# Performance work log

Measured on AMD Instinct MI355X. Metric: run time of the kernel, lower is better.

Reference implementation:

```python
import jax, jax.numpy as jnp
import numpy as np

OUT_DIM = 130

def _gru_cell(x, h, wih, whh, bih, bhh):
    # torch.nn.GRUCell math
    gi = x @ wih.T + bih            # [N, 3H]
    gh = h @ whh.T + bhh            # [N, 3H]
    ir, iz, inn = jnp.split(gi, 3, axis=-1)
    hr, hz, hn = jnp.split(gh, 3, axis=-1)
    r = jax.nn.sigmoid(ir + hr)
    z = jax.nn.sigmoid(iz + hz)
    n = jnp.tanh(inn + r * hn)
    return (1.0 - z) * n + z * h


def setup_inputs() -> dict:
    key = jax.random.key(0)
    ks = jax.random.split(key, 16)
    E, B, C, H, D = 16, 128, 512, 1024, OUT_DIM
    S = 16  # length // 2
    T = E * S
    s = 0.02
    inp = {
        "c": jax.random.normal(ks[0], (E, B, C), jnp.float32),
        "target": jax.random.normal(ks[1], (B, T, D), jnp.float32),
        "length": 32,
        "batch_size": B,
        "fc_init_w": s * jax.random.normal(ks[2], (2 * H, C), jnp.float32),
        "fc_init_b": s * jax.random.normal(ks[3], (2 * H,), jnp.float32),
        "g1_wih": s * jax.random.normal(ks[4], (3 * H, C + D), jnp.float32),
        "g1_whh": s * jax.random.normal(ks[5], (3 * H, H), jnp.float32),
        "g1_bih": s * jax.random.normal(ks[6], (3 * H,), jnp.float32),
        "g1_bhh": s * jax.random.normal(ks[7], (3 * H,), jnp.float32),
        "g2_wih": s * jax.random.normal(ks[8], (3 * H, H), jnp.float32),
        "g2_whh": s * jax.random.normal(ks[9], (3 * H, H), jnp.float32),
        "g2_bih": s * jax.random.normal(ks[10], (3 * H,), jnp.float32),
        "g2_bhh": s * jax.random.normal(ks[11], (3 * H,), jnp.float32),
        "fco_w": s * jax.random.normal(ks[12], (D, H), jnp.float32),
        "fco_b": s * jax.random.normal(ks[13], (D,), jnp.float32),
    }
    return inp


def reference(c, target, length, batch_size, fc_init_w, fc_init_b,
              g1_wih, g1_whh, g1_bih, g1_bhh,
              g2_wih, g2_whh, g2_bih, g2_bhh, fco_w, fco_b):
    E, B, C = c.shape
    H = fc_init_w.shape[0] // 2
    D = fco_w.shape[0]
    S = length // 2
    T = E * S
    # h1/h2 init per conductor embed: tanh(fc_init(embed))
    t0 = jnp.tanh(c @ fc_init_w.T + fc_init_b)           # [E,B,2H]
    h1 = t0[..., :H].reshape(E * B, H)
    h2 = t0[..., H:].reshape(E * B, H)
    # teacher-forced previous: prev[t]=0 at t=0 else target[:,t-1]
    prev = jnp.concatenate([jnp.zeros((B, 1, D), target.dtype), target[:, :T - 1]], axis=1)  # [B,T,D]
    # global step t = e*S + s -> [S, E*B, D]
    prev = prev.transpose(1, 0, 2).reshape(E, S, B, D).transpose(1, 0, 2, 3).reshape(S, E * B, D)
    cflat = c.reshape(E * B, C)

    def step(carry, prev_t):
        h1, h2 = carry
        x = jnp.concatenate([cflat, prev_t], axis=-1)    # [E*B, C+D]
        h1 = _gru_cell(x, h1, g1_wih, g1_whh, g1_bih, g1_bhh)
        h2 = _gru_cell(h1, h2, g2_wih, g2_whh, g2_bih, g2_bhh)
        y = h2 @ fco_w.T + fco_b                         # [E*B, D]
        return (h1, h2), y

    _, ys = jax.lax.scan(step, (h1, h2), prev)           # [S, E*B, D]
    ys = ys.reshape(S, E, B, D).transpose(2, 1, 0, 3).reshape(B, T, D)
    return ys
```

## Files before the change

kernel.cpp:

```cpp
#include <hip/hip_runtime.h>

typedef unsigned short u16;
typedef __attribute__((ext_vector_type(8))) short frag8;
typedef __attribute__((ext_vector_type(4))) float f32x4;
typedef __attribute__((ext_vector_type(8))) unsigned short u16x8;

typedef __attribute__((address_space(1))) const void GV;
typedef __attribute__((address_space(3))) void LV;

__device__ __forceinline__ void gl16(const u16* g, u16* l) {
  __builtin_amdgcn_global_load_lds((GV*)g, (LV*)l, 16, 0, 0);
}

__device__ __forceinline__ float b2f(u16 u) {
  union { unsigned int i; float f; } v; v.i = ((unsigned int)u) << 16; return v.f;
}
__device__ __forceinline__ u16 f2b(float f) {
  union { float f; unsigned int i; } v; v.f = f;
  unsigned int x = v.i;
  x += 0x7fffu + ((x >> 16) & 1u);
  return (u16)(x >> 16);
}
__device__ __forceinline__ float ftanh(float x) {
  float e = __expf(2.f * x);
  return 1.f - 2.f / (e + 1.f);
}

__device__ __forceinline__ void xcd_remap(int axis, int& bx, int& by) {
  const int nx = gridDim.x, ny = gridDim.y;
  const int nwg = nx * ny;
  const int bid = blockIdx.x + nx * blockIdx.y;
  const int q = nwg >> 3, r = nwg & 7;
  const int xcd = bid & 7, i = bid >> 3;
  const int rem = (xcd < r ? xcd * (q + 1) : r * (q + 1) + (xcd - r) * q) + i;
  if (axis == 0) { bx = rem / ny; by = rem - bx * ny; }
  else           { by = rem / nx; bx = rem - by * nx; }
}

__global__ void mega_prep(const float* __restrict__ c, const float* __restrict__ fiw,
                          const float* __restrict__ g1whh, const float* __restrict__ g2wih,
                          const float* __restrict__ g2whh, const float* __restrict__ g1wih,
                          const float* __restrict__ fcow, const float* __restrict__ target,
                          u16* __restrict__ cbf, u16* __restrict__ Wfi, u16* __restrict__ W1h,
                          u16* __restrict__ W2i, u16* __restrict__ W2h, u16* __restrict__ Wc,
                          u16* __restrict__ Wd, u16* __restrict__ WBy, u16* __restrict__ P)
{
  int i = blockIdx.x * 256 + threadIdx.x;
  if (i < 1048576) { cbf[i] = f2b(c[i]); return; }
  i -= 1048576;
  if (i < 1048576) { Wfi[i] = f2b(fiw[i]); return; }
  i -= 1048576;
  if (i < 3145728) { W1h[i] = f2b(g1whh[i]); return; }
  i -= 3145728;
  if (i < 3145728) { W2i[i] = f2b(g2wih[i]); return; }
  i -= 3145728;
  if (i < 3145728) { W2h[i] = f2b(g2whh[i]); return; }
  i -= 3145728;
  if (i < 1572864) { int n = i >> 9, k = i & 511; Wc[i] = f2b(g1wih[n * 642 + k]); return; }
  i -= 1572864;
  if (i < 589824) {
    int n = i / 192, k = i - n * 192;
    Wd[i] = (k < 130) ? f2b(g1wih[n * 642 + 512 + k]) : (u16)0;
    return;
  }
  i -= 589824;
  if (i < 262144) { int n = i >> 10; WBy[i] = (n < 130) ? f2b(fcow[i]) : (u16)0; return; }
  i -= 262144;
  {
    int row = i / 24;
    int k0 = (i - row * 24) * 8;
    int t = row >> 11, m2 = row & 2047;
    int e = m2 >> 7, b = m2 & 127;
    int tt = e * 16 + t;
    u16x8 r;
    if (tt > 0 && k0 + 8 <= 130) {
      const float* trow = target + (size_t)(b * 256 + tt - 1) * 130 + k0;
#pragma unroll
      for (int q = 0; q < 8; ++q) r[q] = f2b(trow[q]);
    } else if (tt > 0 && k0 < 130) {
      const float* trow = target + (size_t)(b * 256 + tt - 1) * 130;
#pragma unroll
      for (int q = 0; q < 8; ++q) { int k = k0 + q; r[q] = (k < 130) ? f2b(trow[k]) : (u16)0; }
    } else {
#pragma unroll
      for (int q = 0; q < 8; ++q) r[q] = (u16)0;
    }
    *(u16x8*)&P[(size_t)row * 192 + k0] = r;
  }
}

__device__ __forceinline__ void kloop3(
    const u16* gA, const u16* gB, int nk,
    u16* AsBase, u16* BsBase, int wave,
    int rdA, int rdB, f32x4 (&acc)[2][4])
{
  u16* Adst = AsBase + wave * 512;
  u16* Bdst = BsBase + wave * 512;
  gl16(gA,      Adst);        gl16(gB,      Bdst);
  gl16(gA + 32, Adst + 4096); gl16(gB + 32, Bdst + 4096);
  const u16* pA = gA + 64;
  const u16* pB = gB + 64;
  int cbuf = 0, nbuf = 2;
  for (int ks = 0; ks < nk; ++ks) {
    if (ks < nk - 1) asm volatile("s_waitcnt vmcnt(2)" : : : "memory");
    else             asm volatile("s_waitcnt vmcnt(0)" : : : "memory");
    __builtin_amdgcn_s_barrier();
    __builtin_amdgcn_sched_barrier(0);
    if (ks + 2 < nk) {
      gl16(pA, Adst + nbuf * 4096);
      gl16(pB, Bdst + nbuf * 4096);
      pA += 32; pB += 32;
    }
    const u16* Ab = AsBase + cbuf * 4096;
    const u16* Bb = BsBase + cbuf * 4096;
    frag8 af[2], bfr[4];
#pragma unroll
    for (int i = 0; i < 2; ++i)
      af[i] = *(const frag8*)&Ab[rdA + i * 512];
#pragma unroll
    for (int j = 0; j < 4; ++j)
      bfr[j] = *(const frag8*)&Bb[rdB + j * 512];
#pragma unroll
    for (int i = 0; i < 2; ++i)
#pragma unroll
      for (int j = 0; j < 4; ++j)
        acc[i][j] = __builtin_amdgcn_mfma_f32_16x16x32_bf16(af[i], bfr[j], acc[i][j], 0, 0, 0);
    cbuf = (cbuf == 2) ? 0 : cbuf + 1;
    nbuf = (nbuf == 2) ? 0 : nbuf + 1;
  }
}

struct GeomT { int wave, lane, wm, wn, lr, lq, rdA, rdB, srow, scol; };
__device__ __forceinline__ GeomT geom(int tid) {
  GeomT g;
  g.wave = tid >> 6; g.lane = tid & 63;
  g.wm = (g.wave & 3) * 32; g.wn = (g.wave >> 2) * 64;
  g.lr = g.lane & 15; g.lq = g.lane >> 4;
  int sw = (g.lr >> 1) & 3;
  g.rdA = (g.wm + g.lr) * 32 + ((g.lq ^ sw) << 3);
  g.rdB = (g.wn + g.lr) * 32 + ((g.lq ^ sw) << 3);
  g.srow = g.wave * 16 + (g.lane >> 2);
  g.scol = (((g.lane & 3) ^ ((g.lane >> 3) & 3)) << 3);
  return g;
}

__global__ __launch_bounds__(512, 6) void gemm_bt(
    const u16* __restrict__ A, int lda,
    const u16* __restrict__ B0, const u16* __restrict__ B1, int ldb, int n_split,
    int N, int K, int mode, int tstep, int axis,
    const float* __restrict__ bias0, const float* __restrict__ bias1,
    u16* __restrict__ out0, u16* __restrict__ out1,
    const u16* __restrict__ addmat,
    float* __restrict__ fout0, float* __restrict__ fout1)
{
  __shared__ u16 As[3 * 4096];
  __shared__ u16 Bs[3 * 4096];
  int bx, by; xcd_remap(axis, bx, by);
  GeomT g = geom(threadIdx.x);
  const int m0 = by * 128, n0 = bx * 128;

  const u16* Bsel; int nb0;
  if (n0 < n_split) { Bsel = B0; nb0 = n0; }
  else              { Bsel = B1; nb0 = n0 - n_split; }

  f32x4 acc[2][4] = {};
  const u16* gA = &A[(size_t)(m0 + g.srow) * lda + g.scol];
  const u16* gB = &Bsel[(size_t)(nb0 + g.srow) * ldb + g.scol];
  kloop3(gA, gB, K >> 5, As, Bs, g.wave, g.rdA, g.rdB, acc);

#pragma unroll
  for (int i = 0; i < 2; ++i) {
#pragma unroll
    for (int r = 0; r < 4; ++r) {
      int m = m0 + g.wm + i * 16 + g.lq * 4 + r;
#pragma unroll
      for (int j = 0; j < 4; ++j) {
        int n = n0 + g.wn + j * 16 + g.lr;
        float v = acc[i][j][r];
        if (mode == 2) {
          out0[(size_t)m * 3072 + n] = f2b(v + b2f(addmat[(size_t)(m & 2047) * 3072 + n]));
        } else if (mode == 3) {
          if (n < 3072) out0[(size_t)m * 3072 + n] = f2b(v + bias0[n]);
          else          out1[(size_t)m * 3072 + (n - 3072)] = f2b(v + bias1[n - 3072]);
        } else {
          if (n < 3072) {
            out0[(size_t)m * 3072 + n] = f2b(v + bias0[n]);
          } else if (n < 3202) {
            int d = n - 3072;
            int b = m & 127, e = m >> 7;
            fout0[(size_t)((b << 8) + (e << 4) + tstep) * 130 + d] = v + bias1[d];
          }
        }
      }
    }
  }
}

__global__ __launch_bounds__(512, 6) void gemm_A(
    const u16* __restrict__ cbf, const u16* __restrict__ Wfi, const u16* __restrict__ Wc,
    const float* __restrict__ fib, const float* __restrict__ g1bih,
    float* __restrict__ h1f, float* __restrict__ h2f,
    u16* __restrict__ h1b, u16* __restrict__ h2b, u16* __restrict__ gic)
{
  __shared__ u16 As[3 * 4096];
  __shared__ u16 Bs[3 * 4096];
  int bx, by; xcd_remap(0, bx, by);
  GeomT g = geom(threadIdx.x);
  const int m0 = by * 128;
  const int isInit = (bx < 16);
  const int nb0 = isInit ? bx * 128 : (bx - 16) * 128;
  const u16* Bw = isInit ? Wfi : Wc;

  f32x4 acc[2][4] = {};
  const u16* gA = &cbf[(size_t)(m0 + g.srow) * 512 + g.scol];
  const u16* gB = &Bw[(size_t)(nb0 + g.srow) * 512 + g.scol];
  kloop3(gA, gB, 16, As, Bs, g.wave, g.rdA, g.rdB, acc);

#pragma unroll
  for (int i = 0; i < 2; ++i) {
#pragma unroll
    for (int r = 0; r < 4; ++r) {
      int m = m0 + g.wm + i * 16 + g.lq * 4 + r;
#pragma unroll
      for (int j = 0; j < 4; ++j) {
        int n = nb0 + g.wn + j * 16 + g.lr;
        float v = acc[i][j][r];
        if (isInit) {
          float t = ftanh(v + fib[n]);
          if (n < 1024) { h1f[(size_t)m * 1024 + n] = t;          h1b[(size_t)m * 1024 + n] = f2b(t); }
          else          { h2f[(size_t)m * 1024 + (n - 1024)] = t; h2b[(size_t)m * 1024 + (n - 1024)] = f2b(t); }
        } else {
          gic[(size_t)m * 3072 + n] = f2b(v + g1bih[n]);
        }
      }
    }
  }
}

__global__ __launch_bounds__(512, 6) void gemm_B(
    const u16* __restrict__ h1b, const u16* __restrict__ h2b, const u16* __restrict__ P,
    const u16* __restrict__ W1h, const u16* __restrict__ W2h, const u16* __restrict__ Wd,
    const float* __restrict__ b1hh, const float* __restrict__ b2hh,
    const u16* __restrict__ gic,
    u16* __restrict__ gh1, u16* __restrict__ gh2, u16* __restrict__ gi1w)
{
  __shared__ u16 As[3 * 4096];
  __shared__ u16 Bs[3 * 4096];
  int bx, by; xcd_remap(0, bx, by);
  GeomT g = geom(threadIdx.x);
  const int m0 = by * 128;
  int reg, nb0;
  const u16 *A, *Bw; int ld, K;
  if (bx < 24)      { reg = 0; nb0 = bx * 128;        A = h1b; Bw = W1h; ld = 1024; K = 1024; }
  else if (bx < 48) { reg = 1; nb0 = (bx - 24) * 128; A = h2b; Bw = W2h; ld = 1024; K = 1024; }
  else              { reg = 2; nb0 = (bx - 48) * 128; A = P;   Bw = Wd;  ld = 192;  K = 192;  }

  f32x4 acc[2][4] = {};
  const u16* gA = &A[(size_t)(m0 + g.srow) * ld + g.scol];
  const u16* gB = &Bw[(size_t)(nb0 + g.srow) * ld + g.scol];
  kloop3(gA, gB, K >> 5, As, Bs, g.wave, g.rdA, g.rdB, acc);

#pragma unroll
  for (int i = 0; i < 2; ++i) {
#pragma unroll
    for (int r = 0; r < 4; ++r) {
      int m = m0 + g.wm + i * 16 + g.lq * 4 + r;
#pragma unroll
      for (int j = 0; j < 4; ++j) {
        int n = nb0 + g.wn + j * 16 + g.lr;
        float v = acc[i][j][r];
        if (reg == 0)      gh1[(size_t)m * 3072 + n] = f2b(v + b1hh[n]);
        else if (reg == 1) gh2[(size_t)m * 3072 + n] = f2b(v + b2hh[n]);
        else               gi1w[(size_t)m * 3072 + n] = f2b(v + b2f(gic[(size_t)m * 3072 + n]));
      }
    }
  }
}

__global__ __launch_bounds__(512, 6) void gemm_fused(
    const u16* __restrict__ h1b, const u16* __restrict__ h2b, const u16* __restrict__ Pt,
    const u16* __restrict__ W2i, const u16* __restrict__ W1h, const u16* __restrict__ W2h,
    const u16* __restrict__ WBy, const u16* __restrict__ Wd,
    const float* __restrict__ b_gi2, const float* __restrict__ b_gh1,
    const float* __restrict__ b_gh2, const float* __restrict__ b_y,
    const u16* __restrict__ gic,
    u16* __restrict__ gi2, u16* __restrict__ gh1, u16* __restrict__ gh2,
    float* __restrict__ y, u16* __restrict__ gi1w,
    int c0, int c1, int c2, int c3, int tstep)
{
  __shared__ u16 As[3 * 4096];
  __shared__ u16 Bs[3 * 4096];
  int bx, by; xcd_remap(0, bx, by);
  GeomT g = geom(threadIdx.x);
  const int m0 = by * 128;
  int reg, nb0;
  const u16 *A, *Bw; int ld, K;
  if (bx < c0)      { reg = 0; nb0 = bx * 128;        A = h1b; Bw = W2i; ld = 1024; K = 1024; }
  else if (bx < c1) { reg = 1; nb0 = (bx - c0) * 128; A = h1b; Bw = W1h; ld = 1024; K = 1024; }
  else if (bx < c2) { reg = 2; nb0 = (bx - c1) * 128; A = h2b; Bw = W2h; ld = 1024; K = 1024; }
  else if (bx < c3) { reg = 3; nb0 = (bx - c2) * 128; A = h2b; Bw = WBy; ld = 1024; K = 1024; }
  else              { reg = 4; nb0 = (bx - c3) * 128; A = Pt;  Bw = Wd;  ld = 192;  K = 192;  }

  f32x4 acc[2][4] = {};
  const u16* gA = &A[(size_t)(m0 + g.srow) * ld + g.scol];
  const u16* gB = &Bw[(size_t)(nb0 + g.srow) * ld + g.scol];
  kloop3(gA, gB, K >> 5, As, Bs, g.wave, g.rdA, g.rdB, acc);

#pragma unroll
  for (int i = 0; i < 2; ++i) {
#pragma unroll
    for (int r = 0; r < 4; ++r) {
      int m = m0 + g.wm + i * 16 + g.lq * 4 + r;
#pragma unroll
      for (int j = 0; j < 4; ++j) {
        int nl = nb0 + g.wn + j * 16 + g.lr;
        float v = acc[i][j][r];
        if (reg == 0)      gi2[(size_t)m * 3072 + nl] = f2b(v + b_gi2[nl]);
        else if (reg == 1) gh1[(size_t)m * 3072 + nl] = f2b(v + b_gh1[nl]);
        else if (reg == 2) gh2[(size_t)m * 3072 + nl] = f2b(v + b_gh2[nl]);
        else if (reg == 3) {
          if (nl < 130) {
            int b = m & 127, e = m >> 7;
            y[(size_t)((b << 8) + (e << 4) + tstep) * 130 + nl] = v + b_y[nl];
          }
        } else {
          gi1w[(size_t)m * 3072 + nl] = f2b(v + b2f(gic[(size_t)m * 3072 + nl]));
        }
      }
    }
  }
}

__global__ __launch_bounds__(256) void gru2(
    const u16* __restrict__ giA, const u16* __restrict__ ghA,
    float* __restrict__ hA, u16* __restrict__ hbA,
    const u16* __restrict__ giB, const u16* __restrict__ ghB,
    float* __restrict__ hB, u16* __restrict__ hbB,
    int doA, int doB)
{
  int blk = blockIdx.x;
  const u16 *gi, *gh; float* h32; u16* hb16;
  if (blk < 1024) { if (!doA) return; gi = giA; gh = ghA; h32 = hA; hb16 = hbA; }
  else { if (!doB) return; gi = giB; gh = ghB; h32 = hB; hb16 = hbB; blk -= 1024; }
  int idx = blk * 256 + threadIdx.x;
  int m = idx >> 7;
  int j0 = (idx & 127) << 3;
  const size_t gb = (size_t)m * 3072 + j0;
  const size_t hb = (size_t)m * 1024 + j0;
  u16x8 ir = *(const u16x8*)&gi[gb];
  u16x8 iz = *(const u16x8*)&gi[gb + 1024];
  u16x8 in_ = *(const u16x8*)&gi[gb + 2048];
  u16x8 hr = *(const u16x8*)&gh[gb];
  u16x8 hz = *(const u16x8*)&gh[gb + 1024];
  u16x8 hn = *(const u16x8*)&gh[gb + 2048];
  f32x4 h0 = *(const f32x4*)&h32[hb];
  f32x4 h1v = *(const f32x4*)&h32[hb + 4];
  f32x4 o0, o1;
  u16x8 ob;
#pragma unroll
  for (int q = 0; q < 8; ++q) {
    float r = 1.f / (1.f + __expf(-(b2f(ir[q]) + b2f(hr[q]))));
    float z = 1.f / (1.f + __expf(-(b2f(iz[q]) + b2f(hz[q]))));
    float nn = ftanh(b2f(in_[q]) + r * b2f(hn[q]));
    float hh = (q < 4) ? h0[q & 3] : h1v[q & 3];
    float res = (1.f - z) * nn + z * hh;
    if (q < 4) o0[q & 3] = res; else o1[q & 3] = res;
    ob[q] = f2b(res);
  }
  *(f32x4*)&h32[hb] = o0;
  *(f32x4*)&h32[hb + 4] = o1;
  *(u16x8*)&hb16[hb] = ob;
}

extern "C" void kernel_launch(void* const* d_in, const int* in_sizes, int n_in,
                              void* d_out, int out_size, void* d_ws, size_t ws_size,
                              hipStream_t stream)
{
  const float* c      = (const float*)d_in[0];
  const float* target = (const float*)d_in[1];
  const float* fiw    = (const float*)d_in[4];
  const float* fib    = (const float*)d_in[5];
  const float* g1wih  = (const float*)d_in[6];
  const float* g1whh  = (const float*)d_in[7];
  const float* g1bih  = (const float*)d_in[8];
  const float* g1bhh  = (const float*)d_in[9];
  const float* g2wih  = (const float*)d_in[10];
  const float* g2whh  = (const float*)d_in[11];
  const float* g2bih  = (const float*)d_in[12];
  const float* g2bhh  = (const float*)d_in[13];
  const float* fcow   = (const float*)d_in[14];
  const float* fcob   = (const float*)d_in[15];
  float* out = (float*)d_out;

  char* wsp = (char*)d_ws;
  size_t off = 0;
  auto takeb = [&](size_t bytes) {
    void* p = (void*)(wsp + off);
    off += bytes;
    off = (off + 255) & ~(size_t)255;
    return p;
  };
  float* h1f = (float*)takeb((size_t)2048 * 1024 * 4);
  float* h2f = (float*)takeb((size_t)2048 * 1024 * 4);
  u16* h1b   = (u16*)takeb((size_t)2048 * 1024 * 2);
  u16* h2b   = (u16*)takeb((size_t)2048 * 1024 * 2);
  u16* gic   = (u16*)takeb((size_t)2048 * 3072 * 2);
  u16* gib   = (u16*)takeb((size_t)2048 * 3072 * 2);
  u16* gh1   = (u16*)takeb((size_t)2048 * 3072 * 2);
  u16* gh2   = (u16*)takeb((size_t)2048 * 3072 * 2);
  u16* cbf   = (u16*)takeb((size_t)2048 * 512 * 2);
  u16* Wfi   = (u16*)takeb((size_t)2048 * 512 * 2);
  u16* Wc    = (u16*)takeb((size_t)3072 * 512 * 2);
  u16* Wd    = (u16*)takeb((size_t)3072 * 192 * 2);
  u16* W1h   = (u16*)takeb((size_t)3072 * 1024 * 2);
  u16* W2i   = (u16*)takeb((size_t)3072 * 1024 * 2);
  u16* W2h   = (u16*)takeb((size_t)3072 * 1024 * 2);
  u16* WBy   = (u16*)takeb((size_t)256 * 1024 * 2);
  u16* P     = (u16*)takeb((size_t)32768 * 192 * 2);
  u16* g1A = nullptr;
  if (ws_size >= off + (size_t)2048 * 3072 * 2 + 256) g1A = (u16*)takeb((size_t)2048 * 3072 * 2);
  (void)in_sizes; (void)n_in; (void)out_size;

  const int BIG = 1 << 30;

  mega_prep<<<57600, 256, 0, stream>>>(c, fiw, g1whh, g2wih, g2whh, g1wih, fcow, target,
                                       cbf, Wfi, W1h, W2i, W2h, Wc, Wd, WBy, P);
  gemm_A<<<dim3(40, 16), 512, 0, stream>>>(cbf, Wfi, Wc, fib, g1bih,
                                           h1f, h2f, h1b, h2b, gic);

  if (g1A != nullptr) {
    gemm_B<<<dim3(72, 16), 512, 0, stream>>>(h1b, h2b, P, W1h, W2h, Wd,
                                             g1bhh, g2bhh, gic, gh1, gh2, g1A);
    gru2<<<2048, 256, 0, stream>>>(g1A, gh1, h1f, h1b, nullptr, nullptr, nullptr, nullptr, 1, 0);
    gemm_fused<<<dim3(72, 16), 512, 0, stream>>>(h1b, h2b, P + (size_t)1 * 2048 * 192,
                                                 W2i, W1h, W2h, WBy, Wd,
                                                 g2bih, g1bhh, g2bhh, fcob, gic,
                                                 gib, gh1, gh2, out, g1A,
                                                 24, 48, 48, 48, 0);
    for (int t = 1; t <= 14; ++t) {
      gru2<<<2048, 256, 0, stream>>>(g1A, gh1, h1f, h1b, gib, gh2, h2f, h2b, 1, 1);
      gemm_fused<<<dim3(98, 16), 512, 0, stream>>>(h1b, h2b, P + (size_t)(t + 1) * 2048 * 192,
                                                   W2i, W1h, W2h, WBy, Wd,
                                                   g2bih, g1bhh, g2bhh, fcob, gic,
                                                   gib, gh1, gh2, out, g1A,
                                                   24, 48, 72, 74, t - 1);
    }
    gru2<<<2048, 256, 0, stream>>>(g1A, gh1, h1f, h1b, gib, gh2, h2f, h2b, 1, 1);
    gemm_fused<<<dim3(50, 16), 512, 0, stream>>>(h1b, h2b, P,
                                                 W2i, W1h, W2h, WBy, Wd,
                                                 g2bih, g1bhh, g2bhh, fcob, gic,
                                                 gib, gh1, gh2, out, g1A,
                                                 24, 24, 48, 50, 14);
    gru2<<<2048, 256, 0, stream>>>(nullptr, nullptr, nullptr, nullptr,
                                   gib, gh2, h2f, h2b, 0, 1);
    gemm_fused<<<dim3(2, 16), 512, 0, stream>>>(h1b, h2b, P,
                                                W2i, W1h, W2h, WBy, Wd,
                                                g2bih, g1bhh, g2bhh, fcob, gic,
                                                gib, gh1, gh2, out, g1A,
                                                0, 0, 0, 2, 15);
  } else {
    gemm_B<<<dim3(48, 16), 512, 0, stream>>>(h1b, h2b, P, W1h, W2h, Wd,
                                             g1bhh, g2bhh, gic, gh1, gh2, nullptr);
    for (int t = 0; t < 16; ++t) {
      gemm_bt<<<dim3(24, 16), 512, 0, stream>>>(P + (size_t)t * 2048 * 192, 192, Wd, nullptr, 192, BIG,
                                                3072, 192, 2, 0, 0, nullptr, nullptr,
                                                gib, nullptr, gic, nullptr, nullptr);
      gru2<<<2048, 256, 0, stream>>>(gib, gh1, h1f, h1b, nullptr, nullptr, nullptr, nullptr, 1, 0);
      gemm_bt<<<dim3(48, 16), 512, 0, stream>>>(h1b, 1024, W2i, W1h, 1024, 3072,
                                                6144, 1024, 3, 0, 0, g2bih, g1bhh,
                                                gib, gh1, nullptr, nullptr, nullptr);
      gru2<<<2048, 256, 0, stream>>>(gib, gh2, h2f, h2b, nullptr, nullptr, nullptr, nullptr, 1, 0);
      gemm_bt<<<dim3(26, 16), 512, 0, stream>>>(h2b, 1024, W2h, WBy, 1024, 3072,
                                                3328, 1024, 4, t, 0, g2bhh, fcob,
                                                gh2, nullptr, nullptr, out, nullptr);
    }
  }
}
```

Measured before the change: 1.803 ms.

## Enlarge GEMM block tile to 256x128 with 64x64 per-wave subtiles

Doubles the M dimension of every GEMM block tile from 128 to 256, with each wave computing a 64x64 output subtile and loading two A row-slices per k-step. The aim is more MFMA work per LDS fragment load and fewer B-matrix reloads across blocks, halving the grid y-dimension. It costs more LDS and accumulator registers per block, lowers occupancy (launch bounds 6 to 4), and reduces the number of blocks available to fill the GPU.

```diff
diff --git a/kernel.cpp b/kernel.cpp
--- a/kernel.cpp
+++ b/kernel.cpp
@@ -90,38 +90,41 @@
 }
 
 __device__ __forceinline__ void kloop3(
-    const u16* gA, const u16* gB, int nk,
+    const u16* gA, int lda, const u16* gB, int nk,
     u16* AsBase, u16* BsBase, int wave,
-    int rdA, int rdB, f32x4 (&acc)[2][4])
-{
-  u16* Adst = AsBase + wave * 512;
-  u16* Bdst = BsBase + wave * 512;
-  gl16(gA,      Adst);        gl16(gB,      Bdst);
-  gl16(gA + 32, Adst + 4096); gl16(gB + 32, Bdst + 4096);
-  const u16* pA = gA + 64;
-  const u16* pB = gB + 64;
+    int rdA, int rdB, f32x4 (&acc)[4][4])
+{
+  u16* Ad = AsBase + wave * 1024;
+  u16* Bd = BsBase + wave * 512;
+  const u16* gA2 = gA + (size_t)16 * lda;
+  gl16(gA,      Ad);            gl16(gA2,      Ad + 512);        gl16(gB,      Bd);
+  gl16(gA + 32, Ad + 8192);     gl16(gA2 + 32, Ad + 8192 + 512); gl16(gB + 32, Bd + 4096);
+  const u16* pA  = gA  + 64;
+  const u16* pA2 = gA2 + 64;
+  const u16* pB  = gB  + 64;
   int cbuf = 0, nbuf = 2;
   for (int ks = 0; ks < nk; ++ks) {
-    if (ks < nk - 1) asm volatile("s_waitcnt vmcnt(2)" : : : "memory");
+    if (ks < nk - 1) asm volatile("s_waitcnt vmcnt(3)" : : : "memory");
     else             asm volatile("s_waitcnt vmcnt(0)" : : : "memory");
     __builtin_amdgcn_s_barrier();
     __builtin_amdgcn_sched_barrier(0);
     if (ks + 2 < nk) {
-      gl16(pA, Adst + nbuf * 4096);
-      gl16(pB, Bdst + nbuf * 4096);
-      pA += 32; pB += 32;
-    }
-    const u16* Ab = AsBase + cbuf * 4096;
+      gl16(pA,  Ad + nbuf * 8192);
+      gl16(pA2, Ad + nbuf * 8192 + 512);
+      gl16(pB,  Bd + nbuf * 4096);
+      pA += 32; pA2 += 32; pB += 32;
+    }
+    const u16* Ab = AsBase + cbuf * 8192;
     const u16* Bb = BsBase + cbuf * 4096;
-    frag8 af[2], bfr[4];
-#pragma unroll
-    for (int i = 0; i < 2; ++i)
+    frag8 af[4], bfr[4];
+#pragma unroll
+    for (int i = 0; i < 4; ++i)
       af[i] = *(const frag8*)&Ab[rdA + i * 512];
 #pragma unroll
     for (int j = 0; j < 4; ++j)
       bfr[j] = *(const frag8*)&Bb[rdB + j * 512];
 #pragma unroll
-    for (int i = 0; i < 2; ++i)
+    for (int i = 0; i < 4; ++i)
 #pragma unroll
       for (int j = 0; j < 4; ++j)
         acc[i][j] = __builtin_amdgcn_mfma_f32_16x16x32_bf16(af[i], bfr[j], acc[i][j], 0, 0, 0);
@@ -130,21 +133,23 @@
   }
 }
 
-struct GeomT { int wave, lane, wm, wn, lr, lq, rdA, rdB, srow, scol; };
+struct GeomT { int wave, lane, wm, wn, lr, lq, rdA, rdB, srowA, srowB, scol; };
 __device__ __forceinline__ GeomT geom(int tid) {
   GeomT g;
   g.wave = tid >> 6; g.lane = tid & 63;
-  g.wm = (g.wave & 3) * 32; g.wn = (g.wave >> 2) * 64;
+  g.wm = (g.wave & 3) * 64;
+  g.wn = (g.wave >> 2) * 64;
   g.lr = g.lane & 15; g.lq = g.lane >> 4;
   int sw = (g.lr >> 1) & 3;
   g.rdA = (g.wm + g.lr) * 32 + ((g.lq ^ sw) << 3);
   g.rdB = (g.wn + g.lr) * 32 + ((g.lq ^ sw) << 3);
-  g.srow = g.wave * 16 + (g.lane >> 2);
+  g.srowA = g.wave * 32 + (g.lane >> 2);
+  g.srowB = g.wave * 16 + (g.lane >> 2);
   g.scol = (((g.lane & 3) ^ ((g.lane >> 3) & 3)) << 3);
   return g;
 }
 
-__global__ __launch_bounds__(512, 6) void gemm_bt(
+__global__ __launch_bounds__(512, 4) void gemm_bt(
     const u16* __restrict__ A, int lda,
     const u16* __restrict__ B0, const u16* __restrict__ B1, int ldb, int n_split,
     int N, int K, int mode, int tstep, int axis,
@@ -153,23 +158,23 @@
     const u16* __restrict__ addmat,
     float* __restrict__ fout0, float* __restrict__ fout1)
 {
-  __shared__ u16 As[3 * 4096];
+  __shared__ u16 As[3 * 8192];
   __shared__ u16 Bs[3 * 4096];
   int bx, by; xcd_remap(axis, bx, by);
   GeomT g = geom(threadIdx.x);
-  const int m0 = by * 128, n0 = bx * 128;
+  const int m0 = by * 256, n0 = bx * 128;
 
   const u16* Bsel; int nb0;
   if (n0 < n_split) { Bsel = B0; nb0 = n0; }
   else              { Bsel = B1; nb0 = n0 - n_split; }
 
-  f32x4 acc[2][4] = {};
-  const u16* gA = &A[(size_t)(m0 + g.srow) * lda + g.scol];
-  const u16* gB = &Bsel[(size_t)(nb0 + g.srow) * ldb + g.scol];
-  kloop3(gA, gB, K >> 5, As, Bs, g.wave, g.rdA, g.rdB, acc);
-
-#pragma unroll
-  for (int i = 0; i < 2; ++i) {
+  f32x4 acc[4][4] = {};
+  const u16* gA = &A[(size_t)(m0 + g.srowA) * lda + g.scol];
+  const u16* gB = &Bsel[(size_t)(nb0 + g.srowB) * ldb + g.scol];
+  kloop3(gA, lda, gB, K >> 5, As, Bs, g.wave, g.rdA, g.rdB, acc);
+
+#pragma unroll
+  for (int i = 0; i < 4; ++i) {
 #pragma unroll
     for (int r = 0; r < 4; ++r) {
       int m = m0 + g.wm + i * 16 + g.lq * 4 + r;
@@ -196,28 +201,28 @@
   }
 }
 
-__global__ __launch_bounds__(512, 6) void gemm_A(
+__global__ __launch_bounds__(512, 4) void gemm_A(
     const u16* __restrict__ cbf, const u16* __restrict__ Wfi, const u16* __restrict__ Wc,
     const float* __restrict__ fib, const float* __restrict__ g1bih,
     float* __restrict__ h1f, float* __restrict__ h2f,
     u16* __restrict__ h1b, u16* __restrict__ h2b, u16* __restrict__ gic)
 {
-  __shared__ u16 As[3 * 4096];
+  __shared__ u16 As[3 * 8192];
   __shared__ u16 Bs[3 * 4096];
   int bx, by; xcd_remap(0, bx, by);
   GeomT g = geom(threadIdx.x);
-  const int m0 = by * 128;
+  const int m0 = by * 256;
   const int isInit = (bx < 16);
   const int nb0 = isInit ? bx * 128 : (bx - 16) * 128;
   const u16* Bw = isInit ? Wfi : Wc;
 
-  f32x4 acc[2][4] = {};
-  const u16* gA = &cbf[(size_t)(m0 + g.srow) * 512 + g.scol];
-  const u16* gB = &Bw[(size_t)(nb0 + g.srow) * 512 + g.scol];
-  kloop3(gA, gB, 16, As, Bs, g.wave, g.rdA, g.rdB, acc);
-
-#pragma unroll
-  for (int i = 0; i < 2; ++i) {
+  f32x4 acc[4][4] = {};
+  const u16* gA = &cbf[(size_t)(m0 + g.srowA) * 512 + g.scol];
+  const u16* gB = &Bw[(size_t)(nb0 + g.srowB) * 512 + g.scol];
+  kloop3(gA, 512, gB, 16, As, Bs, g.wave, g.rdA, g.rdB, acc);
+
+#pragma unroll
+  for (int i = 0; i < 4; ++i) {
 #pragma unroll
     for (int r = 0; r < 4; ++r) {
       int m = m0 + g.wm + i * 16 + g.lq * 4 + r;
@@ -237,31 +242,31 @@
   }
 }
 
-__global__ __launch_bounds__(512, 6) void gemm_B(
+__global__ __launch_bounds__(512, 4) void gemm_B(
     const u16* __restrict__ h1b, const u16* __restrict__ h2b, const u16* __restrict__ P,
     const u16* __restrict__ W1h, const u16* __restrict__ W2h, const u16* __restrict__ Wd,
     const float* __restrict__ b1hh, const float* __restrict__ b2hh,
     const u16* __restrict__ gic,
     u16* __restrict__ gh1, u16* __restrict__ gh2, u16* __restrict__ gi1w)
 {
-  __shared__ u16 As[3 * 4096];
+  __shared__ u16 As[3 * 8192];
   __shared__ u16 Bs[3 * 4096];
   int bx, by; xcd_remap(0, bx, by);
   GeomT g = geom(threadIdx.x);
-  const int m0 = by * 128;
+  const int m0 = by * 256;
   int reg, nb0;
   const u16 *A, *Bw; int ld, K;
   if (bx < 24)      { reg = 0; nb0 = bx * 128;        A = h1b; Bw = W1h; ld = 1024; K = 1024; }
   else if (bx < 48) { reg = 1; nb0 = (bx - 24) * 128; A = h2b; Bw = W2h; ld = 1024; K = 1024; }
   else              { reg = 2; nb0 = (bx - 48) * 128; A = P;   Bw = Wd;  ld = 192;  K = 192;  }
 
-  f32x4 acc[2][4] = {};
-  const u16* gA = &A[(size_t)(m0 + g.srow) * ld + g.scol];
-  const u16* gB = &Bw[(size_t)(nb0 + g.srow) * ld + g.scol];
-  kloop3(gA, gB, K >> 5, As, Bs, g.wave, g.rdA, g.rdB, acc);
-
-#pragma unroll
-  for (int i = 0; i < 2; ++i) {
+  f32x4 acc[4][4] = {};
+  const u16* gA = &A[(size_t)(m0 + g.srowA) * ld + g.scol];
+  const u16* gB = &Bw[(size_t)(nb0 + g.srowB) * ld + g.scol];
+  kloop3(gA, ld, gB, K >> 5, As, Bs, g.wave, g.rdA, g.rdB, acc);
+
+#pragma unroll
+  for (int i = 0; i < 4; ++i) {
 #pragma unroll
     for (int r = 0; r < 4; ++r) {
       int m = m0 + g.wm + i * 16 + g.lq * 4 + r;
@@ -277,7 +282,7 @@
   }
 }
 
-__global__ __launch_bounds__(512, 6) void gemm_fused(
+__global__ __launch_bounds__(512, 4) void gemm_fused(
     const u16* __restrict__ h1b, const u16* __restrict__ h2b, const u16* __restrict__ Pt,
     const u16* __restrict__ W2i, const u16* __restrict__ W1h, const u16* __restrict__ W2h,
     const u16* __restrict__ WBy, const u16* __restrict__ Wd,
@@ -288,11 +293,11 @@
     float* __restrict__ y, u16* __restrict__ gi1w,
     int c0, int c1, int c2, int c3, int tstep)
 {
-  __shared__ u16 As[3 * 4096];
+  __shared__ u16 As[3 * 8192];
   __shared__ u16 Bs[3 * 4096];
   int bx, by; xcd_remap(0, bx, by);
   GeomT g = geom(threadIdx.x);
-  const int m0 = by * 128;
+  const int m0 = by * 256;
   int reg, nb0;
   const u16 *A, *Bw; int ld, K;
   if (bx < c0)      { reg = 0; nb0 = bx * 128;        A = h1b; Bw = W2i; ld = 1024; K = 1024; }
@@ -301,13 +306,13 @@
   else if (bx < c3) { reg = 3; nb0 = (bx - c2) * 128; A = h2b; Bw = WBy; ld = 1024; K = 1024; }
   else              { reg = 4; nb0 = (bx - c3) * 128; A = Pt;  Bw = Wd;  ld = 192;  K = 192;  }
 
-  f32x4 acc[2][4] = {};
-  const u16* gA = &A[(size_t)(m0 + g.srow) * ld + g.scol];
-  const u16* gB = &Bw[(size_t)(nb0 + g.srow) * ld + g.scol];
-  kloop3(gA, gB, K >> 5, As, Bs, g.wave, g.rdA, g.rdB, acc);
-
-#pragma unroll
-  for (int i = 0; i < 2; ++i) {
+  f32x4 acc[4][4] = {};
+  const u16* gA = &A[(size_t)(m0 + g.srowA) * ld + g.scol];
+  const u16* gB = &Bw[(size_t)(nb0 + g.srowB) * ld + g.scol];
+  kloop3(gA, ld, gB, K >> 5, As, Bs, g.wave, g.rdA, g.rdB, acc);
+
+#pragma unroll
+  for (int i = 0; i < 4; ++i) {
 #pragma unroll
     for (int r = 0; r < 4; ++r) {
       int m = m0 + g.wm + i * 16 + g.lq * 4 + r;
@@ -425,54 +430,54 @@
 
   mega_prep<<<57600, 256, 0, stream>>>(c, fiw, g1whh, g2wih, g2whh, g1wih, fcow, target,
                                        cbf, Wfi, W1h, W2i, W2h, Wc, Wd, WBy, P);
-  gemm_A<<<dim3(40, 16), 512, 0, stream>>>(cbf, Wfi, Wc, fib, g1bih,
-                                           h1f, h2f, h1b, h2b, gic);
+  gemm_A<<<dim3(40, 8), 512, 0, stream>>>(cbf, Wfi, Wc, fib, g1bih,
+                                          h1f, h2f, h1b, h2b, gic);
 
   if (g1A != nullptr) {
-    gemm_B<<<dim3(72, 16), 512, 0, stream>>>(h1b, h2b, P, W1h, W2h, Wd,
-                                             g1bhh, g2bhh, gic, gh1, gh2, g1A);
+    gemm_B<<<dim3(72, 8), 512, 0, stream>>>(h1b, h2b, P, W1h, W2h, Wd,
+                                            g1bhh, g2bhh, gic, gh1, gh2, g1A);
     gru2<<<2048, 256, 0, stream>>>(g1A, gh1, h1f, h1b, nullptr, nullptr, nullptr, nullptr, 1, 0);
-    gemm_fused<<<dim3(72, 16), 512, 0, stream>>>(h1b, h2b, P + (size_t)1 * 2048 * 192,
-                                                 W2i, W1h, W2h, WBy, Wd,
-                                                 g2bih, g1bhh, g2bhh, fcob, gic,
-                                                 gib, gh1, gh2, out, g1A,
-                                                 24, 48, 48, 48, 0);
-    for (int t = 1; t <= 14; ++t) {
-      gru2<<<2048, 256, 0, stream>>>(g1A, gh1, h1f, h1b, gib, gh2, h2f, h2b, 1, 1);
-      gemm_fused<<<dim3(98, 16), 512, 0, stream>>>(h1b, h2b, P + (size_t)(t + 1) * 2048 * 192,
-                                                   W2i, W1h, W2h, WBy, Wd,
-                                                   g2bih, g1bhh, g2bhh, fcob, gic,
-                                                   gib, gh1, gh2, out, g1A,
-                                                   24, 48, 72, 74, t - 1);
-    }
-    gru2<<<2048, 256, 0, stream>>>(g1A, gh1, h1f, h1b, gib, gh2, h2f, h2b, 1, 1);
-    gemm_fused<<<dim3(50, 16), 512, 0, stream>>>(h1b, h2b, P,
-                                                 W2i, W1h, W2h, WBy, Wd,
-                                                 g2bih, g1bhh, g2bhh, fcob, gic,
-                                                 gib, gh1, gh2, out, g1A,
-                                                 24, 24, 48, 50, 14);
-    gru2<<<2048, 256, 0, stream>>>(nullptr, nullptr, nullptr, nullptr,
-                                   gib, gh2, h2f, h2b, 0, 1);
-    gemm_fused<<<dim3(2, 16), 512, 0, stream>>>(h1b, h2b, P,
+    gemm_fused<<<dim3(72, 8), 512, 0, stream>>>(h1b, h2b, P + (size_t)1 * 2048 * 192,
                                                 W2i, W1h, W2h, WBy, Wd,
                                                 g2bih, g1bhh, g2bhh, fcob, gic,
                                                 gib, gh1, gh2, out, g1A,
-                                                0, 0, 0, 2, 15);
+                                                24, 48, 48, 48, 0);
+    for (int t = 1; t <= 14; ++t) {
+      gru2<<<2048, 256, 0, stream>>>(g1A, gh1, h1f, h1b, gib, gh2, h2f, h2b, 1, 1);
+      gemm_fused<<<dim3(98, 8), 512, 0, stream>>>(h1b, h2b, P + (size_t)(t + 1) * 2048 * 192,
+                                                  W2i, W1h, W2h, WBy, Wd,
+                                                  g2bih, g1bhh, g2bhh, fcob, gic,
+                                                  gib, gh1, gh2, out, g1A,
+                                                  24, 48, 72, 74, t - 1);
+    }
+    gru2<<<2048, 256, 0, stream>>>(g1A, gh1, h1f, h1b, gib, gh2, h2f, h2b, 1, 1);
+    gemm_fused<<<dim3(50, 8), 512, 0, stream>>>(h1b, h2b, P,
+                                                W2i, W1h, W2h, WBy, Wd,
+                                                g2bih, g1bhh, g2bhh, fcob, gic,
+                                                gib, gh1, gh2, out, g1A,
+                                                24, 24, 48, 50, 14);
+    gru2<<<2048, 256, 0, stream>>>(nullptr, nullptr, nullptr, nullptr,
+                                   gib, gh2, h2f, h2b, 0, 1);
+    gemm_fused<<<dim3(2, 8), 512, 0, stream>>>(h1b, h2b, P,
+                                               W2i, W1h, W2h, WBy, Wd,
+                                               g2bih, g1bhh, g2bhh, fcob, gic,
+                                               gib, gh1, gh2, out, g1A,
+                                               0, 0, 0, 2, 15);
   } else {
-    gemm_B<<<dim3(48, 16), 512, 0, stream>>>(h1b, h2b, P, W1h, W2h, Wd,
-                                             g1bhh, g2bhh, gic, gh1, gh2, nullptr);
+    gemm_B<<<dim3(48, 8), 512, 0, stream>>>(h1b, h2b, P, W1h, W2h, Wd,
+                                            g1bhh, g2bhh, gic, gh1, gh2, nullptr);
     for (int t = 0; t < 16; ++t) {
-      gemm_bt<<<dim3(24, 16), 512, 0, stream>>>(P + (size_t)t * 2048 * 192, 192, Wd, nullptr, 192, BIG,
-                                                3072, 192, 2, 0, 0, nullptr, nullptr,
-                                                gib, nullptr, gic, nullptr, nullptr);
+      gemm_bt<<<dim3(24, 8), 512, 0, stream>>>(P + (size_t)t * 2048 * 192, 192, Wd, nullptr, 192, BIG,
+                                               3072, 192, 2, 0, 0, nullptr, nullptr,
+                                               gib, nullptr, gic, nullptr, nullptr);
       gru2<<<2048, 256, 0, stream>>>(gib, gh1, h1f, h1b, nullptr, nullptr, nullptr, nullptr, 1, 0);
-      gemm_bt<<<dim3(48, 16), 512, 0, stream>>>(h1b, 1024, W2i, W1h, 1024, 3072,
-                                                6144, 1024, 3, 0, 0, g2bih, g1bhh,
-                                                gib, gh1, nullptr, nullptr, nullptr);
+      gemm_bt<<<dim3(48, 8), 512, 0, stream>>>(h1b, 1024, W2i, W1h, 1024, 3072,
+                                               6144, 1024, 3, 0, 0, g2bih, g1bhh,
+                                               gib, gh1, nullptr, nullptr, nullptr);
       gru2<<<2048, 256, 0, stream>>>(gib, gh2, h2f, h2b, nullptr, nullptr, nullptr, nullptr, 1, 0);
-      gemm_bt<<<dim3(26, 16), 512, 0, stream>>>(h2b, 1024, W2h, WBy, 1024, 3072,
-                                                3328, 1024, 4, t, 0, g2bhh, fcob,
-                                                gh2, nullptr, nullptr, out, nullptr);
-    }
-  }
-}
+      gemm_bt<<<dim3(26, 8), 512, 0, stream>>>(h2b, 1024, W2h, WBy, 1024, 3072,
+                                               3328, 1024, 4, t, 0, g2bhh, fcob,
+                                               gh2, nullptr, nullptr, out, nullptr);
+    }
+  }
+}
```

Result: slower. 1.867 ms (+3.6%).
